# Kernel optimization log

Hardware: AMD Instinct MI355X
Metric: run time of the kernel (lower is better)

The kernel has to match this reference:

```python
import jax, jax.numpy as jnp
from jax import lax
import numpy as np

C_IN = 64
C_OUT = 64
CQ = C_OUT // 8   # query/key channels
K = 5             # axial kernel length
RATIO = 0.7       # hybrid-norm mixing ratio
EPS = 1e-5
DN = ('NCHW', 'OIHW', 'NCHW')


def setup_inputs() -> dict:
    key = jax.random.key(0)
    ks = jax.random.split(key, 16)
    rn = lambda k, s, sc=0.05: jax.random.normal(k, s, dtype=jnp.float32) * sc
    return dict(
        x=jax.random.normal(ks[0], (4, C_IN, 256, 256), dtype=jnp.float32),
        hconv_w=rn(ks[1], (C_IN, 1, 1, K)), hconv_b=rn(ks[2], (C_IN,)),
        vconv_w=rn(ks[3], (C_IN, 1, K, 1)), vconv_b=rn(ks[4], (C_IN,)),
        pw_w=rn(ks[5], (C_OUT, C_IN)), pw_b=rn(ks[6], (C_OUT,)),
        bn_w=1.0 + rn(ks[7], (C_OUT,)), bn_b=rn(ks[8], (C_OUT,)),
        q_w=rn(ks[9], (CQ, C_OUT)), q_b=rn(ks[10], (CQ,)),
        k_w=rn(ks[11], (CQ, C_OUT)), k_b=rn(ks[12], (CQ,)),
        v_w=rn(ks[13], (C_OUT, C_OUT)), v_b=rn(ks[14], (C_OUT,)),
        gamma=rn(ks[15], (1,), 0.1),
    )


def reference(x, hconv_w, hconv_b, vconv_w, vconv_b, pw_w, pw_b,
              bn_w, bn_b, q_w, q_b, k_w, k_b, v_w, v_b, gamma):
    # ---- AxialDepthwiseConv: depthwise (1,K) + (K,1) + x, relu, pointwise ----
    h = lax.conv_general_dilated(x, hconv_w, (1, 1), [(0, 0), (K // 2, K // 2)],
                                 dimension_numbers=DN, feature_group_count=C_IN)
    h = h + hconv_b[:, None, None]
    v = lax.conv_general_dilated(x, vconv_w, (1, 1), [(K // 2, K // 2), (0, 0)],
                                 dimension_numbers=DN, feature_group_count=C_IN)
    v = v + vconv_b[:, None, None]
    a = jax.nn.relu(h + v + x)
    y = jnp.einsum('bchw,oc->bohw', a, pw_w) + pw_b[:, None, None]

    # ---- HybridNormalization: 0.7*InstanceNorm(no affine) + 0.3*BatchNorm(train) ----
    im = y.mean((2, 3), keepdims=True)
    iv = y.var((2, 3), keepdims=True)
    inn = (y - im) * lax.rsqrt(iv + EPS)
    bm = y.mean((0, 2, 3), keepdims=True)
    bv = y.var((0, 2, 3), keepdims=True)
    bnn = (y - bm) * lax.rsqrt(bv + EPS) * bn_w[:, None, None] + bn_b[:, None, None]
    y = RATIO * inn + (1.0 - RATIO) * bnn

    # ---- CrissCrossAttention ----
    q = jnp.einsum('bchw,oc->bohw', y, q_w) + q_b[:, None, None]   # (B,CQ,H,W)
    k = jnp.einsum('bchw,oc->bohw', y, k_w) + k_b[:, None, None]   # (B,CQ,H,W)
    val = jnp.einsum('bchw,oc->bohw', y, v_w) + v_b[:, None, None] # (B,C,H,W)

    # height (per column w): attn[b,w,j,i] = softmax_i( q[b,:,j,w] . k[b,:,i,w] )
    Ah = jax.nn.softmax(jnp.einsum('bcjw,bciw->bwji', q, k), axis=-1)
    # h_out[b,c,i,w] = sum_j val[b,c,j,w] * Ah[b,w,j,i]  (matches bmm(value, attn))
    h_out = jnp.einsum('bcjw,bwji->bciw', val, Ah)

    # width (per row h): attn[b,h,y,x] = softmax_x( q[b,:,h,y] . k[b,:,h,x] )
    Av = jax.nn.softmax(jnp.einsum('bchy,bchx->bhyx', q, k), axis=-1)
    v_out = jnp.einsum('bchy,bhyx->bchx', val, Av)

    out = gamma[0] * (h_out + v_out) + y

    # ---- MaxPool2d(2,2) ----
    down = lax.reduce_window(out, -jnp.inf, lax.max, (1, 1, 2, 2), (1, 1, 2, 2), 'VALID')
    return out, down
```

## Files before the change

### kernel.cpp

```cpp
#include <hip/hip_runtime.h>
#include <hip/hip_bf16.h>

#define Bn 4
#define Cc 64
#define CQn 8
#define Hh 256
#define Ww 256
#define PLANE 65536

typedef unsigned short ushortT;
typedef __attribute__((ext_vector_type(8))) unsigned short us8;
typedef __attribute__((ext_vector_type(4))) unsigned short us4;
typedef __attribute__((ext_vector_type(8))) __bf16 bf16x8;
typedef __attribute__((ext_vector_type(4))) float f32x4;

__device__ inline ushortT f2bf(float f) {
    __hip_bfloat16 h = __float2bfloat16(f);
    return *(ushortT*)&h;
}
__device__ inline float bf2f(ushortT u) {
    return __uint_as_float((unsigned)u << 16);
}
union BF8U { us8 u; bf16x8 b; uint4 w; };
__device__ inline us8 zero_us8() {
    BF8U z; z.w.x = 0; z.w.y = 0; z.w.z = 0; z.w.w = 0; return z.u;
}

__global__ void pack_weights_kernel(
    const float* __restrict__ pww, const float* __restrict__ qw,
    const float* __restrict__ kw, const float* __restrict__ vw,
    ushortT* __restrict__ pw_bf, ushortT* __restrict__ qk_bf,
    ushortT* __restrict__ vw_bf)
{
    int i = blockIdx.x * 256 + threadIdx.x;
    if (i < 64 * 64) pw_bf[i] = f2bf(pww[i]);
    if (i < 64 * 64) vw_bf[i] = f2bf(vw[i]);
    if (i < 8 * 64)  qk_bf[i] = f2bf(qw[i]);
    if (i >= 8 * 64 && i < 16 * 64) qk_bf[i] = f2bf(kw[i - 512]);
}

__global__ __launch_bounds__(256) void dw_kernel(
    const float* __restrict__ x,
    const float* __restrict__ hw, const float* __restrict__ hb,
    const float* __restrict__ vw, const float* __restrict__ vb,
    ushortT* __restrict__ aout)
{
    int blk = blockIdx.x;
    int bc = blk >> 4;
    int ht = blk & 15;
    int h0 = ht * 16;
    int c = bc & 63;
    int tid = threadIdx.x;
    __shared__ float rows[20][260];
    const float* xp = x + (size_t)bc * PLANE;
    #pragma unroll
    for (int i = 0; i < 20; ++i) {
        int hr = h0 - 2 + i;
        rows[i][tid + 2] = (hr >= 0 && hr < Hh) ? xp[hr * Ww + tid] : 0.f;
    }
    if (tid < 20) {
        rows[tid][0] = 0.f; rows[tid][1] = 0.f;
        rows[tid][258] = 0.f; rows[tid][259] = 0.f;
    }
    __syncthreads();

    float hw0 = hw[c * 5 + 0], hw1 = hw[c * 5 + 1], hw2 = hw[c * 5 + 2],
          hw3 = hw[c * 5 + 3], hw4 = hw[c * 5 + 4];
    float vw0 = vw[c * 5 + 0], vw1 = vw[c * 5 + 1], vw2 = vw[c * 5 + 2],
          vw3 = vw[c * 5 + 3], vw4 = vw[c * 5 + 4];
    float bias = hb[c] + vb[c];

    ushortT* op = aout + (size_t)bc * PLANE + h0 * Ww + tid;
    #pragma unroll
    for (int r = 0; r < 16; ++r) {
        float hs = hw0 * rows[r + 2][tid]     + hw1 * rows[r + 2][tid + 1]
                 + hw2 * rows[r + 2][tid + 2] + hw3 * rows[r + 2][tid + 3]
                 + hw4 * rows[r + 2][tid + 4];
        float vs = vw0 * rows[r][tid + 2]     + vw1 * rows[r + 1][tid + 2]
                 + vw2 * rows[r + 2][tid + 2] + vw3 * rows[r + 3][tid + 2]
                 + vw4 * rows[r + 4][tid + 2];
        float res = hs + vs + bias + rows[r + 2][tid + 2];
        op[r * Ww] = f2bf(fmaxf(res, 0.f));
    }
}

__global__ __launch_bounds__(256) void pw_mfma_kernel(
    const ushortT* __restrict__ a_bf, const ushortT* __restrict__ pw_bf,
    const float* __restrict__ pwb,
    float* __restrict__ y_raw, float* __restrict__ sums, float* __restrict__ sumsq)
{
    int blk = blockIdx.x;
    int b = blk >> 8;
    int t0 = (blk & 255) << 8;
    int tid = threadIdx.x, lane = tid & 63, wv = tid >> 6;
    int half = lane >> 4;
    int col = lane & 15;

    __shared__ ushortT ytile[256 * 74];

    {
        size_t base = (size_t)b * Cc * PLANE + t0 + tid;
        uint* wrow = (uint*)&ytile[tid * 74];
        #pragma unroll
        for (int c = 0; c < Cc; c += 2) {
            ushortT v0 = a_bf[base + (size_t)c * PLANE];
            ushortT v1 = a_bf[base + (size_t)(c + 1) * PLANE];
            wrow[c >> 1] = (uint)v0 | ((uint)v1 << 16);
        }
    }
    __syncthreads();

    int m0 = wv * 16;
    BF8U a0, a1;
    a0.u = *(const us8*)(pw_bf + (m0 + col) * 64 + half * 8);
    a1.u = *(const us8*)(pw_bf + (m0 + col) * 64 + 32 + half * 8);

    float bias[4], s[4], s2[4];
    #pragma unroll
    for (int r = 0; r < 4; ++r) {
        bias[r] = pwb[m0 + half * 4 + r];
        s[r] = 0.f; s2[r] = 0.f;
    }

    const uint* lw = (const uint*)ytile;
    #pragma unroll 4
    for (int t = 0; t < 16; ++t) {
        int rbase = (t * 16 + col) * 37 + half * 4;
        BF8U b0, b1;
        b0.w.x = lw[rbase];      b0.w.y = lw[rbase + 1];
        b0.w.z = lw[rbase + 2];  b0.w.w = lw[rbase + 3];
        b1.w.x = lw[rbase + 16]; b1.w.y = lw[rbase + 17];
        b1.w.z = lw[rbase + 18]; b1.w.w = lw[rbase + 19];
        f32x4 acc = (f32x4){0.f, 0.f, 0.f, 0.f};
        acc = __builtin_amdgcn_mfma_f32_16x16x32_bf16(a0.b, b0.b, acc, 0, 0, 0);
        acc = __builtin_amdgcn_mfma_f32_16x16x32_bf16(a1.b, b1.b, acc, 0, 0, 0);
        int pix = t * 16 + col;
        #pragma unroll
        for (int r = 0; r < 4; ++r) {
            int c = m0 + half * 4 + r;
            float v = acc[r] + bias[r];
            y_raw[(size_t)(b * Cc + c) * PLANE + t0 + pix] = v;
            s[r] += v; s2[r] += v * v;
        }
    }
    #pragma unroll
    for (int r = 0; r < 4; ++r) {
        #pragma unroll
        for (int d = 8; d > 0; d >>= 1) {
            s[r]  += __shfl_down(s[r], d, 16);
            s2[r] += __shfl_down(s2[r], d, 16);
        }
    }
    if (col == 0) {
        #pragma unroll
        for (int r = 0; r < 4; ++r) {
            int c = m0 + half * 4 + r;
            atomicAdd(&sums[b * Cc + c], s[r]);
            atomicAdd(&sumsq[b * Cc + c], s2[r]);
        }
    }
}

__global__ __launch_bounds__(256) void qkv_mfma_kernel(
    const float* __restrict__ y_raw,
    const float* __restrict__ sums, const float* __restrict__ sumsq,
    const float* __restrict__ bnw, const float* __restrict__ bnb,
    const ushortT* __restrict__ qk_bf, const float* __restrict__ qbias,
    const float* __restrict__ kbias,
    const ushortT* __restrict__ vw_bf, const float* __restrict__ vbias,
    float* __restrict__ y_norm, ushortT* __restrict__ q, ushortT* __restrict__ k,
    ushortT* __restrict__ val)
{
    int blk = blockIdx.x;
    int b = blk >> 8;
    int t0 = (blk & 255) << 8;
    int tid = threadIdx.x, lane = tid & 63, wv = tid >> 6;
    int half = lane >> 4;
    int col = lane & 15;

    __shared__ ushortT ytile[256 * 74];
    __shared__ float alpha_s[64], beta_s[64];

    if (tid < 64) {
        int c = tid;
        float im[4], e2[4];
        float bm = 0.f, be2 = 0.f;
        #pragma unroll
        for (int bb = 0; bb < 4; ++bb) {
            im[bb] = sums[bb * Cc + c] * (1.f / 65536.f);
            e2[bb] = sumsq[bb * Cc + c] * (1.f / 65536.f);
            bm += im[bb]; be2 += e2[bb];
        }
        bm *= 0.25f; be2 *= 0.25f;
        float rsb = rsqrtf(be2 - bm * bm + 1e-5f);
        float wgt = bnw[c];
        float rsi = rsqrtf(e2[b] - im[b] * im[b] + 1e-5f);
        alpha_s[c] = 0.7f * rsi + 0.3f * rsb * wgt;
        beta_s[c]  = -0.7f * im[b] * rsi - 0.3f * bm * rsb * wgt + 0.3f * bnb[c];
    }
    __syncthreads();

    {
        size_t base = (size_t)b * Cc * PLANE + t0 + tid;
        uint* wrow = (uint*)&ytile[tid * 74];
        #pragma unroll
        for (int c = 0; c < Cc; c += 2) {
            float v0 = y_raw[base + (size_t)c * PLANE];
            float v1 = y_raw[base + (size_t)(c + 1) * PLANE];
            float n0 = alpha_s[c] * v0 + beta_s[c];
            float n1 = alpha_s[c + 1] * v1 + beta_s[c + 1];
            y_norm[base + (size_t)c * PLANE] = n0;
            y_norm[base + (size_t)(c + 1) * PLANE] = n1;
            wrow[c >> 1] = (uint)f2bf(n0) | ((uint)f2bf(n1) << 16);
        }
    }
    __syncthreads();

    const uint* lw = (const uint*)ytile;

    {
        BF8U a0, a1;
        a0.u = *(const us8*)(qk_bf + col * 64 + half * 8);
        a1.u = *(const us8*)(qk_bf + col * 64 + 32 + half * 8);
        #pragma unroll
        for (int i = 0; i < 4; ++i) {
            int t = wv * 4 + i;
            int rbase = (t * 16 + col) * 37 + half * 4;
            BF8U b0, b1;
            b0.w.x = lw[rbase];      b0.w.y = lw[rbase + 1];
            b0.w.z = lw[rbase + 2];  b0.w.w = lw[rbase + 3];
            b1.w.x = lw[rbase + 16]; b1.w.y = lw[rbase + 17];
            b1.w.z = lw[rbase + 18]; b1.w.w = lw[rbase + 19];
            f32x4 acc = (f32x4){0.f, 0.f, 0.f, 0.f};
            acc = __builtin_amdgcn_mfma_f32_16x16x32_bf16(a0.b, b0.b, acc, 0, 0, 0);
            acc = __builtin_amdgcn_mfma_f32_16x16x32_bf16(a1.b, b1.b, acc, 0, 0, 0);
            int pix = t * 16 + col;
            #pragma unroll
            for (int r = 0; r < 4; ++r) {
                int row = half * 4 + r;
                if (row < 8)
                    q[(size_t)(b * CQn + row) * PLANE + t0 + pix] = f2bf(acc[r] + qbias[row]);
                else
                    k[(size_t)(b * CQn + row - 8) * PLANE + t0 + pix] = f2bf(acc[r] + kbias[row - 8]);
            }
        }
    }

    {
        int m0 = wv * 16;
        BF8U a0, a1;
        a0.u = *(const us8*)(vw_bf + (m0 + col) * 64 + half * 8);
        a1.u = *(const us8*)(vw_bf + (m0 + col) * 64 + 32 + half * 8);
        float bias[4];
        #pragma unroll
        for (int r = 0; r < 4; ++r) bias[r] = vbias[m0 + half * 4 + r];
        #pragma unroll 4
        for (int t = 0; t < 16; ++t) {
            int rbase = (t * 16 + col) * 37 + half * 4;
            BF8U b0, b1;
            b0.w.x = lw[rbase];      b0.w.y = lw[rbase + 1];
            b0.w.z = lw[rbase + 2];  b0.w.w = lw[rbase + 3];
            b1.w.x = lw[rbase + 16]; b1.w.y = lw[rbase + 17];
            b1.w.z = lw[rbase + 18]; b1.w.w = lw[rbase + 19];
            f32x4 acc = (f32x4){0.f, 0.f, 0.f, 0.f};
            acc = __builtin_amdgcn_mfma_f32_16x16x32_bf16(a0.b, b0.b, acc, 0, 0, 0);
            acc = __builtin_amdgcn_mfma_f32_16x16x32_bf16(a1.b, b1.b, acc, 0, 0, 0);
            int pix = t * 16 + col;
            #pragma unroll
            for (int r = 0; r < 4; ++r) {
                int c = m0 + half * 4 + r;
                val[(size_t)(b * Cc + c) * PLANE + t0 + pix] = f2bf(acc[r] + bias[r]);
            }
        }
    }
}

__global__ __launch_bounds__(256) void transpose_all_kernel(
    const ushortT* __restrict__ qb, ushortT* __restrict__ qT,
    const ushortT* __restrict__ kb, ushortT* __restrict__ kT,
    const ushortT* __restrict__ vb, ushortT* __restrict__ vT)
{
    int blk = blockIdx.x;
    int plane = blk >> 6;
    int tile = blk & 63;
    const ushortT* src; ushortT* dst;
    if (plane < 32)      { src = qb + (size_t)plane * PLANE;        dst = qT + (size_t)plane * PLANE; }
    else if (plane < 64) { src = kb + (size_t)(plane - 32) * PLANE; dst = kT + (size_t)(plane - 32) * PLANE; }
    else                 { src = vb + (size_t)(plane - 64) * PLANE; dst = vT + (size_t)(plane - 64) * PLANE; }
    int th = (tile >> 3) * 32;
    int tw = (tile & 7) * 32;
    __shared__ ushortT t[32][34];
    int lw = threadIdx.x & 31;
    int lh = threadIdx.x >> 5;
    #pragma unroll
    for (int i = 0; i < 4; ++i)
        t[lh + 8 * i][lw] = src[(th + lh + 8 * i) * Ww + tw + lw];
    __syncthreads();
    #pragma unroll
    for (int i = 0; i < 4; ++i)
        dst[(tw + lh + 8 * i) * Hh + th + lw] = t[lw][lh + 8 * i];
}

__global__ __launch_bounds__(256) void attn_kernel(
    const ushortT* __restrict__ q0, const ushortT* __restrict__ k0,
    const ushortT* __restrict__ v0, ushortT* __restrict__ o0,
    const ushortT* __restrict__ q1, const ushortT* __restrict__ k1,
    const ushortT* __restrict__ v1, ushortT* __restrict__ o1)
{
    int blk = blockIdx.x;
    int sel = blk >> 10;
    const ushortT* __restrict__ q   = sel ? q1 : q0;
    const ushortT* __restrict__ k   = sel ? k1 : k0;
    const ushortT* __restrict__ val = sel ? v1 : v0;
    ushortT* __restrict__ outp      = sel ? o1 : o0;
    int bblk = blk & 1023;
    int b = bblk >> 8;
    int r = bblk & 255;
    int tid = threadIdx.x;
    int lane = tid & 63;
    int wv = tid >> 6;
    int col = lane & 15;
    int quad = lane >> 4;

    __shared__ ushortT q_s[256 * 8];
    __shared__ ushortT k_s[256 * 8];
    __shared__ ushortT A_lds[4 * 256 * 8];
    __shared__ float mhat[256];
    __shared__ float shiftv[256];
    __shared__ float kred[32];

    size_t vbase = (size_t)b * Cc * PLANE + (size_t)r * Ww
                 + (size_t)(wv * 16 + col) * PLANE + quad * 8;
    BF8U afb[2];
    afb[0].u = *(const us8*)(val + vbase);

    size_t qkbase = (size_t)b * CQn * PLANE + (size_t)r * Ww + tid;
    float qf[8], ka[8];
    {
        BF8U qp, kp;
        #pragma unroll
        for (int c = 0; c < 8; ++c) {
            ushortT qv = q[qkbase + (size_t)c * PLANE];
            ushortT kv = k[qkbase + (size_t)c * PLANE];
            qp.u[c] = qv; kp.u[c] = kv;
            qf[c] = bf2f(qv);
            ka[c] = fabsf(bf2f(kv));
        }
        *(us8*)&q_s[tid * 8] = qp.u;
        *(us8*)&k_s[tid * 8] = kp.u;
    }
    #pragma unroll
    for (int d = 1; d < 64; d <<= 1)
        #pragma unroll
        for (int c = 0; c < 8; ++c)
            ka[c] = fmaxf(ka[c], __shfl_xor(ka[c], d));
    if (lane == 0)
        #pragma unroll
        for (int c = 0; c < 8; ++c) kred[wv * 8 + c] = ka[c];
    __syncthreads();

    {
        float mh = 0.f;
        #pragma unroll
        for (int c = 0; c < 8; ++c) {
            float km = fmaxf(fmaxf(kred[c], kred[8 + c]),
                             fmaxf(kred[16 + c], kred[24 + c]));
            mh += fabsf(qf[c]) * km;
        }
        mhat[tid] = mh;
    }
    __syncthreads();

    #pragma unroll
    for (int t = 0; t < 4; ++t) {
        int jt = wv * 4 + t;
        BF8U qa; qa.u = zero_us8();
        if (quad == 0) qa.u = *(const us8*)&q_s[(jt * 16 + col) * 8];
        float mh4[4];
        #pragma unroll
        for (int rr = 0; rr < 4; ++rr) mh4[rr] = mhat[jt * 16 + quad * 4 + rr];
        f32x4 ls = (f32x4){0.f, 0.f, 0.f, 0.f};
        for (int it = 0; it < 16; ++it) {
            BF8U kb;
            kb.u = *(const us8*)&k_s[(it * 16 + col) * 8];
            f32x4 sacc = (f32x4){0.f, 0.f, 0.f, 0.f};
            sacc = __builtin_amdgcn_mfma_f32_16x16x32_bf16(qa.b, kb.b, sacc, 0, 0, 0);
            #pragma unroll
            for (int rr = 0; rr < 4; ++rr)
                ls[rr] += __expf(sacc[rr] - mh4[rr]);
        }
        #pragma unroll
        for (int d = 1; d < 16; d <<= 1)
            #pragma unroll
            for (int rr = 0; rr < 4; ++rr)
                ls[rr] += __shfl_xor(ls[rr], d);
        if (col == 0)
            #pragma unroll
            for (int rr = 0; rr < 4; ++rr)
                shiftv[jt * 16 + quad * 4 + rr] = mh4[rr] + __logf(ls[rr]);
    }
    __syncthreads();

    BF8U kc[4];
    #pragma unroll
    for (int i = 0; i < 4; ++i)
        kc[i].u = *(const us8*)&k_s[((wv * 4 + i) * 16 + col) * 8];
    f32x4 acc[16];
    #pragma unroll
    for (int t = 0; t < 16; ++t) acc[t] = (f32x4){0.f, 0.f, 0.f, 0.f};

    #pragma unroll
    for (int ks = 0; ks < 8; ++ks) {
        if (ks < 7)
            afb[(ks + 1) & 1].u = *(const us8*)(val + vbase + (ks + 1) * 32);
        #pragma unroll
        for (int jj2 = 0; jj2 < 2; ++jj2) {
            int jt = ks * 2 + jj2;
            BF8U qa; qa.u = zero_us8();
            if (quad == 0) qa.u = *(const us8*)&q_s[(jt * 16 + col) * 8];
            float sh4[4];
            #pragma unroll
            for (int rr = 0; rr < 4; ++rr) sh4[rr] = shiftv[jt * 16 + quad * 4 + rr];
            #pragma unroll
            for (int i = 0; i < 4; ++i) {
                f32x4 sacc = (f32x4){0.f, 0.f, 0.f, 0.f};
                sacc = __builtin_amdgcn_mfma_f32_16x16x32_bf16(qa.b, kc[i].b, sacc, 0, 0, 0);
                us4 pk;
                #pragma unroll
                for (int rr = 0; rr < 4; ++rr)
                    pk[rr] = f2bf(__expf(sacc[rr] - sh4[rr]));
                int irow = (wv * 4 + i) * 16 + col;
                int jq = jj2 * 2 + (quad >> 1);
                *(us4*)&A_lds[(jq * 256 + irow) * 8 + (quad & 1) * 4] = pk;
            }
        }
        __syncthreads();
        #pragma unroll
        for (int t = 0; t < 16; ++t) {
            BF8U bfr;
            bfr.u = *(const us8*)&A_lds[(quad * 256 + t * 16 + col) * 8];
            acc[t] = __builtin_amdgcn_mfma_f32_16x16x32_bf16(afb[ks & 1].b, bfr.b, acc[t], 0, 0, 0);
        }
        __syncthreads();
    }

    size_t obase = (size_t)b * Cc * PLANE + (size_t)r * Ww;
    #pragma unroll
    for (int t = 0; t < 16; ++t) {
        int i = t * 16 + col;
        #pragma unroll
        for (int rr = 0; rr < 4; ++rr) {
            int c = wv * 16 + quad * 4 + rr;
            outp[obase + (size_t)c * PLANE + i] = f2bf(acc[t][rr]);
        }
    }
}

__global__ __launch_bounds__(256) void final_kernel(
    const ushortT* __restrict__ houtT, const ushortT* __restrict__ hout0,
    const float* __restrict__ y_norm, const float* __restrict__ gamma,
    float* __restrict__ out, float* __restrict__ down)
{
    int blk = blockIdx.x;
    int tile = blk & 63;
    int bc = blk >> 6;
    int th = (tile >> 3) * 32;
    int tw = (tile & 7) * 32;
    __shared__ float t[32][33];
    const ushortT* hT = houtT + (size_t)bc * PLANE;
    {
        int ww = threadIdx.x >> 3;
        int hh = (threadIdx.x & 7) * 4;
        us4 v4 = *(const us4*)(hT + (size_t)(tw + ww) * Hh + th + hh);
        t[hh + 0][ww] = __uint_as_float((unsigned)v4[0] << 16);
        t[hh + 1][ww] = __uint_as_float((unsigned)v4[1] << 16);
        t[hh + 2][ww] = __uint_as_float((unsigned)v4[2] << 16);
        t[hh + 3][ww] = __uint_as_float((unsigned)v4[3] << 16);
    }
    __syncthreads();
    float g = gamma[0];
    int qw_ = threadIdx.x & 15;
    int qh_ = threadIdx.x >> 4;
    const float* yb = y_norm + (size_t)bc * PLANE;
    const ushortT* hb = hout0 + (size_t)bc * PLANE;
    float* ob = out + (size_t)bc * PLANE;
    float mx = -1e30f;
    float2 res[2];
    #pragma unroll
    for (int i = 0; i < 2; ++i) {
        int hh = 2 * qh_ + i;
        int off = (th + hh) * Ww + tw + 2 * qw_;
        uint hv = *(const uint*)(hb + off);
        float2 y = *(const float2*)(yb + off);
        float o0 = g * (t[hh][2 * qw_]     + bf2f((ushortT)(hv & 0xffff))) + y.x;
        float o1 = g * (t[hh][2 * qw_ + 1] + bf2f((ushortT)(hv >> 16)))   + y.y;
        res[i] = make_float2(o0, o1);
        mx = fmaxf(mx, fmaxf(o0, o1));
    }
    #pragma unroll
    for (int i = 0; i < 2; ++i) {
        int off = (th + 2 * qh_ + i) * Ww + tw + 2 * qw_;
        *(float2*)(ob + off) = res[i];
    }
    down[(size_t)bc * 16384 + (th / 2 + qh_) * 128 + tw / 2 + qw_] = mx;
}

extern "C" void kernel_launch(void* const* d_in, const int* in_sizes, int n_in,
                              void* d_out, int out_size, void* d_ws, size_t ws_size,
                              hipStream_t stream)
{
    const float* x     = (const float*)d_in[0];
    const float* hw    = (const float*)d_in[1];
    const float* hb    = (const float*)d_in[2];
    const float* vw    = (const float*)d_in[3];
    const float* vb    = (const float*)d_in[4];
    const float* pww   = (const float*)d_in[5];
    const float* pwb   = (const float*)d_in[6];
    const float* bnw   = (const float*)d_in[7];
    const float* bnb   = (const float*)d_in[8];
    const float* qw    = (const float*)d_in[9];
    const float* qb    = (const float*)d_in[10];
    const float* kw    = (const float*)d_in[11];
    const float* kb    = (const float*)d_in[12];
    const float* vw2   = (const float*)d_in[13];
    const float* vb2   = (const float*)d_in[14];
    const float* gamma = (const float*)d_in[15];

    float* ws = (float*)d_ws;
    const size_t NP = (size_t)Bn * Cc * PLANE;
    const size_t NQ = (size_t)Bn * CQn * PLANE;
    float* y_raw  = ws;
    float* y_norm = ws + NP;
    float* slotC  = ws + 2 * NP;
    float* slotD  = ws + 2 * NP + NP / 2;
    float* ptr    = ws + 3 * NP;
    ushortT* qbuf = (ushortT*)ptr;
    ushortT* kbuf = qbuf + NQ;
    ushortT* qT   = kbuf + NQ;
    ushortT* kT   = qT + NQ;
    float* sums   = (float*)(kT + NQ);
    float* sumsq  = sums + 256;
    ushortT* pw_bf = (ushortT*)(sumsq + 256);
    ushortT* qk_bf = pw_bf + 64 * 64;
    ushortT* vw_bf = qk_bf + 16 * 64;

    ushortT* a_buf = (ushortT*)slotC;
    ushortT* valT  = (ushortT*)slotC;
    ushortT* valb  = (ushortT*)slotD;
    ushortT* hout0 = (ushortT*)y_raw;
    ushortT* houtT = hout0 + NP;
    float* out  = (float*)d_out;
    float* down = out + NP;

    hipMemsetAsync(sums, 0, 512 * sizeof(float), stream);
    pack_weights_kernel<<<dim3(16), dim3(256), 0, stream>>>(
        pww, qw, kw, vw2, pw_bf, qk_bf, vw_bf);
    dw_kernel<<<dim3(Bn * Cc * 16), dim3(256), 0, stream>>>(
        x, hw, hb, vw, vb, a_buf);
    pw_mfma_kernel<<<dim3(Bn * 256), dim3(256), 0, stream>>>(
        a_buf, pw_bf, pwb, y_raw, sums, sumsq);
    qkv_mfma_kernel<<<dim3(Bn * 256), dim3(256), 0, stream>>>(
        y_raw, sums, sumsq, bnw, bnb, qk_bf, qb, kb, vw_bf, vb2,
        y_norm, qbuf, kbuf, valb);
    transpose_all_kernel<<<dim3(320 * 64), dim3(256), 0, stream>>>(
        qbuf, qT, kbuf, kT, valb, valT);
    attn_kernel<<<dim3(2 * Bn * Hh), dim3(256), 0, stream>>>(
        qbuf, kbuf, valb, hout0, qT, kT, valT, houtT);
    final_kernel<<<dim3(Bn * Cc * 64), dim3(256), 0, stream>>>(
        houtT, hout0, y_norm, gamma, out, down);
}
```

Before: 371.6 us.

## Fold softmax normalization into value operand and recompute y_norm in final kernel

Removes the separate softmax-denominator pass in the attention kernel. Exp sums are now accumulated during the main pass, reduced across waves through shared memory, and applied as reciprocal scales on the value fragment before the MFMA. The log2e factor is folded into q so exp2 can be used. It also stops writing the fp32 y_norm tensor and instead recomputes the normalization affine from y_raw in the final kernel, saving a full fp32 write and read. This adds an extra barrier-free reduction per k-step, and scaling bf16 values before rounding may change precision slightly.

After: 370.8 us. Within noise of the previous version (-0.2%).

```diff
diff --git a/kernel.cpp b/kernel.cpp
--- a/kernel.cpp
+++ b/kernel.cpp
@@ -7,6 +7,7 @@
 #define Hh 256
 #define Ww 256
 #define PLANE 65536
+#define LOG2E 1.4426950408889634f
 
 typedef unsigned short ushortT;
 typedef __attribute__((ext_vector_type(8))) unsigned short us8;
@@ -168,7 +169,7 @@
     const ushortT* __restrict__ qk_bf, const float* __restrict__ qbias,
     const float* __restrict__ kbias,
     const ushortT* __restrict__ vw_bf, const float* __restrict__ vbias,
-    float* __restrict__ y_norm, ushortT* __restrict__ q, ushortT* __restrict__ k,
+    ushortT* __restrict__ q, ushortT* __restrict__ k,
     ushortT* __restrict__ val)
 {
     int blk = blockIdx.x;
@@ -209,8 +210,6 @@
             float v1 = y_raw[base + (size_t)(c + 1) * PLANE];
             float n0 = alpha_s[c] * v0 + beta_s[c];
             float n1 = alpha_s[c + 1] * v1 + beta_s[c + 1];
-            y_norm[base + (size_t)c * PLANE] = n0;
-            y_norm[base + (size_t)(c + 1) * PLANE] = n1;
             wrow[c >> 1] = (uint)f2bf(n0) | ((uint)f2bf(n1) << 16);
         }
     }
@@ -239,7 +238,8 @@
             for (int r = 0; r < 4; ++r) {
                 int row = half * 4 + r;
                 if (row < 8)
-                    q[(size_t)(b * CQn + row) * PLANE + t0 + pix] = f2bf(acc[r] + qbias[row]);
+                    q[(size_t)(b * CQn + row) * PLANE + t0 + pix] =
+                        f2bf((acc[r] + qbias[row]) * LOG2E);
                 else
                     k[(size_t)(b * CQn + row - 8) * PLANE + t0 + pix] = f2bf(acc[r] + kbias[row - 8]);
             }
@@ -326,8 +326,8 @@
     __shared__ ushortT k_s[256 * 8];
     __shared__ ushortT A_lds[4 * 256 * 8];
     __shared__ float mhat[256];
-    __shared__ float shiftv[256];
     __shared__ float kred[32];
+    __shared__ float lsum[4][32];
 
     size_t vbase = (size_t)b * Cc * PLANE + (size_t)r * Ww
                  + (size_t)(wv * 16 + col) * PLANE + quad * 8;
@@ -371,36 +371,6 @@
     }
     __syncthreads();
 
-    #pragma unroll
-    for (int t = 0; t < 4; ++t) {
-        int jt = wv * 4 + t;
-        BF8U qa; qa.u = zero_us8();
-        if (quad == 0) qa.u = *(const us8*)&q_s[(jt * 16 + col) * 8];
-        float mh4[4];
-        #pragma unroll
-        for (int rr = 0; rr < 4; ++rr) mh4[rr] = mhat[jt * 16 + quad * 4 + rr];
-        f32x4 ls = (f32x4){0.f, 0.f, 0.f, 0.f};
-        for (int it = 0; it < 16; ++it) {
-            BF8U kb;
-            kb.u = *(const us8*)&k_s[(it * 16 + col) * 8];
-            f32x4 sacc = (f32x4){0.f, 0.f, 0.f, 0.f};
-            sacc = __builtin_amdgcn_mfma_f32_16x16x32_bf16(qa.b, kb.b, sacc, 0, 0, 0);
-            #pragma unroll
-            for (int rr = 0; rr < 4; ++rr)
-                ls[rr] += __expf(sacc[rr] - mh4[rr]);
-        }
-        #pragma unroll
-        for (int d = 1; d < 16; d <<= 1)
-            #pragma unroll
-            for (int rr = 0; rr < 4; ++rr)
-                ls[rr] += __shfl_xor(ls[rr], d);
-        if (col == 0)
-            #pragma unroll
-            for (int rr = 0; rr < 4; ++rr)
-                shiftv[jt * 16 + quad * 4 + rr] = mh4[rr] + __logf(ls[rr]);
-    }
-    __syncthreads();
-
     BF8U kc[4];
     #pragma unroll
     for (int i = 0; i < 4; ++i)
@@ -413,33 +383,64 @@
     for (int ks = 0; ks < 8; ++ks) {
         if (ks < 7)
             afb[(ks + 1) & 1].u = *(const us8*)(val + vbase + (ks + 1) * 32);
+        float ps[8];
+        #pragma unroll
+        for (int e = 0; e < 8; ++e) ps[e] = 0.f;
         #pragma unroll
         for (int jj2 = 0; jj2 < 2; ++jj2) {
             int jt = ks * 2 + jj2;
             BF8U qa; qa.u = zero_us8();
             if (quad == 0) qa.u = *(const us8*)&q_s[(jt * 16 + col) * 8];
-            float sh4[4];
+            float mh4[4];
             #pragma unroll
-            for (int rr = 0; rr < 4; ++rr) sh4[rr] = shiftv[jt * 16 + quad * 4 + rr];
+            for (int rr = 0; rr < 4; ++rr) mh4[rr] = mhat[jt * 16 + quad * 4 + rr];
             #pragma unroll
             for (int i = 0; i < 4; ++i) {
                 f32x4 sacc = (f32x4){0.f, 0.f, 0.f, 0.f};
                 sacc = __builtin_amdgcn_mfma_f32_16x16x32_bf16(qa.b, kc[i].b, sacc, 0, 0, 0);
                 us4 pk;
                 #pragma unroll
-                for (int rr = 0; rr < 4; ++rr)
-                    pk[rr] = f2bf(__expf(sacc[rr] - sh4[rr]));
+                for (int rr = 0; rr < 4; ++rr) {
+                    float e = __builtin_amdgcn_exp2f(sacc[rr] - mh4[rr]);
+                    ps[jj2 * 4 + rr] += e;
+                    pk[rr] = f2bf(e);
+                }
                 int irow = (wv * 4 + i) * 16 + col;
                 int jq = jj2 * 2 + (quad >> 1);
                 *(us4*)&A_lds[(jq * 256 + irow) * 8 + (quad & 1) * 4] = pk;
             }
         }
+        #pragma unroll
+        for (int d = 1; d < 16; d <<= 1)
+            #pragma unroll
+            for (int e = 0; e < 8; ++e)
+                ps[e] += __shfl_xor(ps[e], d);
+        if (col == 0) {
+            #pragma unroll
+            for (int jj2 = 0; jj2 < 2; ++jj2)
+                #pragma unroll
+                for (int rr = 0; rr < 4; ++rr)
+                    lsum[wv][jj2 * 16 + quad * 4 + rr] = ps[jj2 * 4 + rr];
+        }
         __syncthreads();
+        f32x4 l0 = *(const f32x4*)&lsum[0][quad * 8];
+        f32x4 l1 = *(const f32x4*)&lsum[0][quad * 8 + 4];
+        #pragma unroll
+        for (int w = 1; w < 4; ++w) {
+            l0 += *(const f32x4*)&lsum[w][quad * 8];
+            l1 += *(const f32x4*)&lsum[w][quad * 8 + 4];
+        }
+        BF8U av;
+        #pragma unroll
+        for (int e = 0; e < 4; ++e) {
+            av.u[e]     = f2bf(bf2f(afb[ks & 1].u[e])     * __builtin_amdgcn_rcpf(l0[e]));
+            av.u[4 + e] = f2bf(bf2f(afb[ks & 1].u[4 + e]) * __builtin_amdgcn_rcpf(l1[e]));
+        }
         #pragma unroll
         for (int t = 0; t < 16; ++t) {
             BF8U bfr;
             bfr.u = *(const us8*)&A_lds[(quad * 256 + t * 16 + col) * 8];
-            acc[t] = __builtin_amdgcn_mfma_f32_16x16x32_bf16(afb[ks & 1].b, bfr.b, acc[t], 0, 0, 0);
+            acc[t] = __builtin_amdgcn_mfma_f32_16x16x32_bf16(av.b, bfr.b, acc[t], 0, 0, 0);
         }
         __syncthreads();
     }
@@ -458,14 +459,35 @@
 
 __global__ __launch_bounds__(256) void final_kernel(
     const ushortT* __restrict__ houtT, const ushortT* __restrict__ hout0,
-    const float* __restrict__ y_norm, const float* __restrict__ gamma,
+    const float* __restrict__ y_raw,
+    const float* __restrict__ sums, const float* __restrict__ sumsq,
+    const float* __restrict__ bnw, const float* __restrict__ bnb,
+    const float* __restrict__ gamma,
     float* __restrict__ out, float* __restrict__ down)
 {
     int blk = blockIdx.x;
     int tile = blk & 63;
     int bc = blk >> 6;
+    int b = bc >> 6;
+    int c = bc & 63;
     int th = (tile >> 3) * 32;
     int tw = (tile & 7) * 32;
+
+    float im[4], e2[4];
+    float bm = 0.f, be2 = 0.f;
+    #pragma unroll
+    for (int bb = 0; bb < 4; ++bb) {
+        im[bb] = sums[bb * Cc + c] * (1.f / 65536.f);
+        e2[bb] = sumsq[bb * Cc + c] * (1.f / 65536.f);
+        bm += im[bb]; be2 += e2[bb];
+    }
+    bm *= 0.25f; be2 *= 0.25f;
+    float rsb = rsqrtf(be2 - bm * bm + 1e-5f);
+    float wgt = bnw[c];
+    float rsi = rsqrtf(e2[b] - im[b] * im[b] + 1e-5f);
+    float al = 0.7f * rsi + 0.3f * rsb * wgt;
+    float bt = -0.7f * im[b] * rsi - 0.3f * bm * rsb * wgt + 0.3f * bnb[c];
+
     __shared__ float t[32][33];
     const ushortT* hT = houtT + (size_t)bc * PLANE;
     {
@@ -481,7 +503,7 @@
     float g = gamma[0];
     int qw_ = threadIdx.x & 15;
     int qh_ = threadIdx.x >> 4;
-    const float* yb = y_norm + (size_t)bc * PLANE;
+    const float* yb = y_raw + (size_t)bc * PLANE;
     const ushortT* hb = hout0 + (size_t)bc * PLANE;
     float* ob = out + (size_t)bc * PLANE;
     float mx = -1e30f;
@@ -492,8 +514,10 @@
         int off = (th + hh) * Ww + tw + 2 * qw_;
         uint hv = *(const uint*)(hb + off);
         float2 y = *(const float2*)(yb + off);
-        float o0 = g * (t[hh][2 * qw_]     + bf2f((ushortT)(hv & 0xffff))) + y.x;
-        float o1 = g * (t[hh][2 * qw_ + 1] + bf2f((ushortT)(hv >> 16)))   + y.y;
+        float y0 = al * y.x + bt;
+        float y1 = al * y.y + bt;
+        float o0 = g * (t[hh][2 * qw_]     + bf2f((ushortT)(hv & 0xffff))) + y0;
+        float o1 = g * (t[hh][2 * qw_ + 1] + bf2f((ushortT)(hv >> 16)))   + y1;
         res[i] = make_float2(o0, o1);
         mx = fmaxf(mx, fmaxf(o0, o1));
     }
@@ -530,7 +554,7 @@
     const size_t NP = (size_t)Bn * Cc * PLANE;
     const size_t NQ = (size_t)Bn * CQn * PLANE;
     float* y_raw  = ws;
-    float* y_norm = ws + NP;
+    float* slotB  = ws + NP;
     float* slotC  = ws + 2 * NP;
     float* slotD  = ws + 2 * NP + NP / 2;
     float* ptr    = ws + 3 * NP;
@@ -547,7 +571,7 @@
     ushortT* a_buf = (ushortT*)slotC;
     ushortT* valT  = (ushortT*)slotC;
     ushortT* valb  = (ushortT*)slotD;
-    ushortT* hout0 = (ushortT*)y_raw;
+    ushortT* hout0 = (ushortT*)slotB;
     ushortT* houtT = hout0 + NP;
     float* out  = (float*)d_out;
     float* down = out + NP;
@@ -561,11 +585,11 @@
         a_buf, pw_bf, pwb, y_raw, sums, sumsq);
     qkv_mfma_kernel<<<dim3(Bn * 256), dim3(256), 0, stream>>>(
         y_raw, sums, sumsq, bnw, bnb, qk_bf, qb, kb, vw_bf, vb2,
-        y_norm, qbuf, kbuf, valb);
+        qbuf, kbuf, valb);
     transpose_all_kernel<<<dim3(320 * 64), dim3(256), 0, stream>>>(
         qbuf, qT, kbuf, kT, valb, valT);
     attn_kernel<<<dim3(2 * Bn * Hh), dim3(256), 0, stream>>>(
         qbuf, kbuf, valb, hout0, qT, kT, valT, houtT);
     final_kernel<<<dim3(Bn * Cc * 64), dim3(256), 0, stream>>>(
-        houtT, hout0, y_norm, gamma, out, down);
-}
+        houtT, hout0, y_raw, sums, sumsq, bnw, bnb, gamma, out, down);
+}
```
